# Performance work log

Measured on AMD Instinct MI355X. Metric: run time of the kernel, lower is better.

The kernel has to match this reference:

```python
import jax, jax.numpy as jnp
import numpy as np

B, N, D, H = 8, 1024, 768, 12
HD = D // H


def setup_inputs() -> dict:
    key = jax.random.key(0)
    ks = jax.random.split(key, 9)
    s = 1.0 / np.sqrt(D)
    return {
        "x": jax.random.normal(ks[0], (B, N, D), dtype=jnp.float32),
        "Wq": jax.random.normal(ks[1], (D, D), dtype=jnp.float32) * s,
        "bq": jax.random.normal(ks[2], (D,), dtype=jnp.float32) * 0.01,
        "Wk": jax.random.normal(ks[3], (D, D), dtype=jnp.float32) * s,
        "bk": jax.random.normal(ks[4], (D,), dtype=jnp.float32) * 0.01,
        "Wv": jax.random.normal(ks[5], (D, D), dtype=jnp.float32) * s,
        "bv": jax.random.normal(ks[6], (D,), dtype=jnp.float32) * 0.01,
        "Wo": jax.random.normal(ks[7], (D, D), dtype=jnp.float32) * s,
        "bo": jax.random.normal(ks[8], (D,), dtype=jnp.float32) * 0.01,
    }


def reference(x, Wq, bq, Wk, bk, Wv, bv, Wo, bo):
    b, n, d = x.shape
    split = lambda t: t.reshape(b, n, H, HD).transpose(0, 2, 1, 3)  # b h n d
    q = split(x @ Wq + bq)
    k = split(x @ Wk + bk)
    v = split(x @ Wv + bv)
    energy = jnp.einsum('bhqd,bhkd->bhqk', q, k)
    # NOTE: module scales AFTER softmax by sqrt(emb_size) (not head_dim) -- faithful.
    att = jax.nn.softmax(energy, axis=-1) / jnp.sqrt(jnp.float32(D)).astype(x.dtype)
    out = jnp.einsum('bhqk,bhkd->bhqd', att, v)
    out = out.transpose(0, 2, 1, 3).reshape(b, n, d)
    return out @ Wo + bo
```

## Files before the change

kernel.cpp:

```cpp
#include <hip/hip_runtime.h>

#define B_  8
#define N_  1024
#define D_  768
#define H_  12
#define HD_ 64
#define M_  (B_ * N_)
#define WELEM (D_ * D_)
#define XELEM ((size_t)M_ * D_)

typedef _Float16 f16;
typedef f16   f16x8  __attribute__((ext_vector_type(8)));
typedef short bf16x8 __attribute__((ext_vector_type(8)));
typedef float f32x4  __attribute__((ext_vector_type(4)));
typedef unsigned short u16;

__device__ __forceinline__ u16 f2bf(float f) {
    unsigned int x = __float_as_uint(f);
    return (u16)((x + 0x7fffu + ((x >> 16) & 1u)) >> 16);
}
__device__ __forceinline__ u16 f2h(float f) {
    return __builtin_bit_cast(u16, (f16)f);
}
__device__ __forceinline__ unsigned int cvtpk_bf16(float lo, float hi) {
    unsigned int r;
    asm("v_cvt_pk_bf16_f32 %0, %1, %2" : "=v"(r) : "v"(lo), "v"(hi));
    return r;
}
#if __has_builtin(__builtin_amdgcn_exp2f)
#define EXP2F(x) __builtin_amdgcn_exp2f(x)
#else
#define EXP2F(x) exp2f(x)
#endif

#define LOG2E_   1.4426950408889634f
#define EXPBIAS_ 28.853900817779268f

typedef __attribute__((address_space(3))) unsigned int       as3_u32;
typedef __attribute__((address_space(1))) const unsigned int as1_u32;
__device__ __forceinline__ void dma16(const void* g, void* l) {
    __builtin_amdgcn_global_load_lds((as1_u32*)g, (as3_u32*)l, 16, 0, 0);
}

__global__ __launch_bounds__(256) void cvt_x(const float* __restrict__ X,
                                             u16* __restrict__ Xh) {
    int idx = blockIdx.x * 256 + threadIdx.x;
    float4 v = ((const float4*)X)[idx];
    ushort4 o = {f2h(v.x), f2h(v.y), f2h(v.z), f2h(v.w)};
    ((ushort4*)Xh)[idx] = o;
}

__global__ __launch_bounds__(256) void cvt_w(
    const float* __restrict__ w0, const float* __restrict__ w1,
    const float* __restrict__ w2, const float* __restrict__ w3,
    u16* __restrict__ Wt) {
    const float* W = blockIdx.y == 0 ? w0 : blockIdx.y == 1 ? w1
                   : blockIdx.y == 2 ? w2 : w3;
    u16* dst = Wt + (size_t)blockIdx.y * WELEM;
    const int t  = threadIdx.x;
    const int tk = (blockIdx.x % 12) * 64, tn = (blockIdx.x / 12) * 64;
    __shared__ __align__(16) float tile[64][68];
#pragma unroll
    for (int i = 0; i < 4; ++i) {
        int r = (t >> 4) + i * 16, c4 = (t & 15) * 4;
        float4 v = *(const float4*)(W + (size_t)(tk + r) * D_ + tn + c4);
        *(float4*)&tile[r][c4] = v;
    }
    __syncthreads();
#pragma unroll
    for (int i = 0; i < 4; ++i) {
        int nr = (t >> 4) + i * 16, kc = (t & 15) * 4;
        ushort4 o = {f2h(tile[kc + 0][nr]), f2h(tile[kc + 1][nr]),
                     f2h(tile[kc + 2][nr]), f2h(tile[kc + 3][nr])};
        *(ushort4*)(dst + (size_t)(tn + nr) * D_ + tk + kc) = o;
    }
}

__global__ __launch_bounds__(256) void gemm_qkv(
    const u16* __restrict__ Xh, const u16* __restrict__ Wt,
    const float* __restrict__ bq, const float* __restrict__ bk,
    const float* __restrict__ bv, u16* __restrict__ Qf,
    u16* __restrict__ Kf, u16* __restrict__ Vt) {
    __shared__ __align__(16) u16 As[128 * 64];
    __shared__ __align__(16) u16 Bs[128 * 64];

    const int id  = blockIdx.x;
    const int xcd = id & 7, idx = id >> 3;
    const int m0  = (xcd * 8 + idx / 18) * 128;
    const int rem = idx % 18;
    const int z   = rem / 6, n0 = (rem % 6) * 128;

    const u16* Wz = Wt + (size_t)z * WELEM;
    const float* bias = z == 0 ? bq : z == 1 ? bk : bv;

    const int t = threadIdx.x, lane = t & 63, w = t >> 6;
    const int wm = w >> 1, wn = w & 1;
    const int quad = lane >> 4, ln = lane & 15;
    const int drow = lane >> 3, dcl = (lane & 7) ^ ((lane >> 3) & 7);

    f32x4 acc[4][4] = {};
    for (int k0 = 0; k0 < D_; k0 += 64) {
        __syncthreads();
#pragma unroll
        for (int j = 0; j < 4; ++j) {
            int i = w * 4 + j, row = i * 8 + drow;
            dma16(Xh + (size_t)(m0 + row) * D_ + k0 + dcl * 8, &As[i * 512]);
        }
#pragma unroll
        for (int j = 0; j < 4; ++j) {
            int i = w * 4 + j, row = i * 8 + drow;
            dma16(Wz + (size_t)(n0 + row) * D_ + k0 + dcl * 8, &Bs[i * 512]);
        }
        __syncthreads();
        f16x8 a[4][2], b[4][2];
#pragma unroll
        for (int mt = 0; mt < 4; ++mt)
#pragma unroll
            for (int ks = 0; ks < 2; ++ks)
                a[mt][ks] = *(const f16x8*)&As[(wm * 64 + mt * 16 + ln) * 64 +
                                               (((ks * 4 + quad) ^ (ln & 7)) * 8)];
#pragma unroll
        for (int nt = 0; nt < 4; ++nt)
#pragma unroll
            for (int ks = 0; ks < 2; ++ks)
                b[nt][ks] = *(const f16x8*)&Bs[(wn * 64 + nt * 16 + ln) * 64 +
                                               (((ks * 4 + quad) ^ (ln & 7)) * 8)];
#pragma unroll
        for (int mt = 0; mt < 4; ++mt)
#pragma unroll
            for (int nt = 0; nt < 4; ++nt) {
                acc[mt][nt] = __builtin_amdgcn_mfma_f32_16x16x32_f16(
                    a[mt][0], b[nt][0], acc[mt][nt], 0, 0, 0);
                acc[mt][nt] = __builtin_amdgcn_mfma_f32_16x16x32_f16(
                    a[mt][1], b[nt][1], acc[mt][nt], 0, 0, 0);
            }
    }
    const int h = (n0 >> 6) + wn;
#pragma unroll
    for (int nt = 0; nt < 4; ++nt) {
        int hd = nt * 16 + ln;
        float bv_ = bias[n0 + wn * 64 + hd];
#pragma unroll
        for (int mt = 0; mt < 4; ++mt) {
            int mb = m0 + wm * 64 + mt * 16 + quad * 4;
            int bb = mb >> 10, ns = mb & 1023;
            if (z == 0) {
#pragma unroll
                for (int r = 0; r < 4; ++r)
                    Qf[(((size_t)bb * H_ + h) * N_ + ns + r) * HD_ + hd] =
                        f2h((acc[mt][nt][r] + bv_) * LOG2E_);
            } else if (z == 1) {
#pragma unroll
                for (int r = 0; r < 4; ++r)
                    Kf[(((size_t)bb * H_ + h) * N_ + ns + r) * HD_ + hd] =
                        f2h(acc[mt][nt][r] + bv_);
            } else {
                ushort4 o = {f2bf(acc[mt][nt][0] + bv_), f2bf(acc[mt][nt][1] + bv_),
                             f2bf(acc[mt][nt][2] + bv_), f2bf(acc[mt][nt][3] + bv_)};
                *(ushort4*)(Vt + (((size_t)bb * H_ + h) * HD_ + hd) * N_ + ns) = o;
            }
        }
    }
}

__global__ __launch_bounds__(256) void attn_mfma(
    const u16* __restrict__ Qg, const u16* __restrict__ Kg,
    const u16* __restrict__ Vtg, u16* __restrict__ Og) {
    __shared__ __align__(16) u16 Ks[2][64 * 64];
    __shared__ __align__(16) u16 Vs[2][64 * 64];
    __shared__ __align__(16) u16 Ps[128 * 72];

    const int t = threadIdx.x, lane = t & 63, w = t >> 6;
    const int quad = lane >> 4, ln = lane & 15;
    const int drow = lane >> 3, dcl = (lane & 7) ^ ((lane >> 3) & 7);
    const int id  = blockIdx.x;
    const int id2 = (id & 7) * 96 + (id >> 3);
    const int bh  = id2 >> 3, qt = id2 & 7;
    const u16* Qh  = Qg  + ((size_t)bh * N_ + qt * 128) * HD_;
    const u16* Kh  = Kg  + (size_t)bh * N_ * HD_;
    const u16* Vth = Vtg + (size_t)bh * HD_ * N_;
    u16*       Oh  = Og  + ((size_t)bh * N_ + qt * 128) * HD_;

    const int rho0 = (w * 2 + 0) * 8 + drow;
    const int rho1 = (w * 2 + 1) * 8 + drow;
    const int gk0  = 4 * (rho0 & 15) + (rho0 >> 4);
    const int gk1  = 4 * (rho1 & 15) + (rho1 >> 4);

    f16x8 aq[2][2];
#pragma unroll
    for (int mt = 0; mt < 2; ++mt)
#pragma unroll
        for (int ks = 0; ks < 2; ++ks)
            aq[mt][ks] = *(const f16x8*)(Qh + (size_t)(w * 32 + mt * 16 + ln) * HD_ +
                                         ks * 32 + quad * 8);

    const bf16x8 pone = {0x3F80, 0x3F80, 0x3F80, 0x3F80,
                         0x3F80, 0x3F80, 0x3F80, 0x3F80};
    const f32x4 nb = {-EXPBIAS_, -EXPBIAS_, -EXPBIAS_, -EXPBIAS_};

    f32x4 oacc[2][4] = {};
    f32x4 lacc[2] = {};

    dma16(Kh + (size_t)gk0 * HD_ + dcl * 8, &Ks[0][(w * 2 + 0) * 512]);
    dma16(Kh + (size_t)gk1 * HD_ + dcl * 8, &Ks[0][(w * 2 + 1) * 512]);
    dma16(Vth + (size_t)rho0 * N_ + dcl * 8, &Vs[0][(w * 2 + 0) * 512]);
    dma16(Vth + (size_t)rho1 * N_ + dcl * 8, &Vs[0][(w * 2 + 1) * 512]);

#pragma unroll 2
    for (int kt = 0; kt < 16; ++kt) {
        const int cur = kt & 1;
        asm volatile("s_waitcnt vmcnt(0)" ::: "memory");
        __builtin_amdgcn_s_barrier();
        __builtin_amdgcn_sched_barrier(0);
        if (kt < 15) {
            const int nk = (kt + 1) * 64;
            dma16(Kh + (size_t)(nk + gk0) * HD_ + dcl * 8, &Ks[cur ^ 1][(w * 2 + 0) * 512]);
            dma16(Kh + (size_t)(nk + gk1) * HD_ + dcl * 8, &Ks[cur ^ 1][(w * 2 + 1) * 512]);
            dma16(Vth + (size_t)rho0 * N_ + nk + dcl * 8, &Vs[cur ^ 1][(w * 2 + 0) * 512]);
            dma16(Vth + (size_t)rho1 * N_ + nk + dcl * 8, &Vs[cur ^ 1][(w * 2 + 1) * 512]);
        }

        f32x4 sf[2][4];
        __builtin_amdgcn_s_setprio(1);
#pragma unroll
        for (int nt = 0; nt < 4; ++nt) {
            f16x8 b0 = *(const f16x8*)&Ks[cur][(nt * 16 + ln) * 64 + ((quad) ^ (ln & 7)) * 8];
            f16x8 b1 = *(const f16x8*)&Ks[cur][(nt * 16 + ln) * 64 + ((4 + quad) ^ (ln & 7)) * 8];
#pragma unroll
            for (int mt = 0; mt < 2; ++mt) {
                sf[mt][nt] = __builtin_amdgcn_mfma_f32_16x16x32_f16(aq[mt][0], b0, nb, 0, 0, 0);
                sf[mt][nt] = __builtin_amdgcn_mfma_f32_16x16x32_f16(aq[mt][1], b1, sf[mt][nt], 0, 0, 0);
            }
        }
        __builtin_amdgcn_s_setprio(0);

#pragma unroll
        for (int mt = 0; mt < 2; ++mt)
#pragma unroll
            for (int r = 0; r < 4; ++r) {
                float e0 = EXP2F(sf[mt][0][r]);
                float e1 = EXP2F(sf[mt][1][r]);
                float e2 = EXP2F(sf[mt][2][r]);
                float e3 = EXP2F(sf[mt][3][r]);
                uint2 pk;
                pk.x = cvtpk_bf16(e0, e1);
                pk.y = cvtpk_bf16(e2, e3);
                int q = w * 32 + mt * 16 + quad * 4 + r;
                *(uint2*)&Ps[q * 72 + ln * 4] = pk;
            }

        __builtin_amdgcn_s_setprio(1);
#pragma unroll
        for (int mt = 0; mt < 2; ++mt) {
            bf16x8 ap0 = *(const bf16x8*)&Ps[(w * 32 + mt * 16 + ln) * 72 + quad * 8];
            bf16x8 ap1 = *(const bf16x8*)&Ps[(w * 32 + mt * 16 + ln) * 72 + 32 + quad * 8];
            lacc[mt] = __builtin_amdgcn_mfma_f32_16x16x32_bf16(ap0, pone, lacc[mt], 0, 0, 0);
            lacc[mt] = __builtin_amdgcn_mfma_f32_16x16x32_bf16(ap1, pone, lacc[mt], 0, 0, 0);
#pragma unroll
            for (int nt = 0; nt < 4; ++nt) {
                bf16x8 bv0 = *(const bf16x8*)&Vs[cur][(nt * 16 + ln) * 64 +
                                                      ((quad ^ (ln & 7)) * 8)];
                oacc[mt][nt] = __builtin_amdgcn_mfma_f32_16x16x32_bf16(
                    ap0, bv0, oacc[mt][nt], 0, 0, 0);
                bf16x8 bv1 = *(const bf16x8*)&Vs[cur][(nt * 16 + ln) * 64 +
                                                      (((4 + quad) ^ (ln & 7)) * 8)];
                oacc[mt][nt] = __builtin_amdgcn_mfma_f32_16x16x32_bf16(
                    ap1, bv1, oacc[mt][nt], 0, 0, 0);
            }
        }
        __builtin_amdgcn_s_setprio(0);
    }

    const float sc = 0.036084391824351615f;
#pragma unroll
    for (int mt = 0; mt < 2; ++mt)
#pragma unroll
        for (int r = 0; r < 4; ++r) {
            float inv = sc / lacc[mt][r];
#pragma unroll
            for (int nt = 0; nt < 4; ++nt)
                Oh[(size_t)(w * 32 + mt * 16 + quad * 4 + r) * HD_ + nt * 16 + ln] =
                    f2h(oacc[mt][nt][r] * inv);
        }
}

__global__ __launch_bounds__(256) void gemm_out(
    const u16* __restrict__ Ob, const u16* __restrict__ Wto,
    const float* __restrict__ bias, float* __restrict__ Out) {
    __shared__ __align__(16) u16 As[128 * 64];
    __shared__ __align__(16) u16 Bs[64 * 64];

    const int id  = blockIdx.x;
    const int id2 = (id & 7) * 96 + (id >> 3);
    const int m0  = (id2 / 12) * 128, n0 = (id2 % 12) * 64;

    const int t = threadIdx.x, lane = t & 63, w = t >> 6;
    const int wm = w >> 1, wn = w & 1;
    const int quad = lane >> 4, ln = lane & 15;
    const int drow = lane >> 3, dcl = (lane & 7) ^ ((lane >> 3) & 7);

    f32x4 acc[4][2] = {};
    for (int k0 = 0; k0 < D_; k0 += 64) {
        int head = k0 >> 6;
        __syncthreads();
#pragma unroll
        for (int j = 0; j < 4; ++j) {
            int i = w * 4 + j, row = i * 8 + drow;
            int m = m0 + row, bb = m >> 10, ns = m & 1023;
            dma16(Ob + (((size_t)bb * H_ + head) * N_ + ns) * HD_ + dcl * 8, &As[i * 512]);
        }
#pragma unroll
        for (int j = 0; j < 2; ++j) {
            int i = w * 2 + j, row = i * 8 + drow;
            dma16(Wto + (size_t)(n0 + row) * D_ + k0 + dcl * 8, &Bs[i * 512]);
        }
        __syncthreads();
        f16x8 a[4][2], b[2][2];
#pragma unroll
        for (int mt = 0; mt < 4; ++mt)
#pragma unroll
            for (int ks = 0; ks < 2; ++ks)
                a[mt][ks] = *(const f16x8*)&As[(wm * 64 + mt * 16 + ln) * 64 +
                                               (((ks * 4 + quad) ^ (ln & 7)) * 8)];
#pragma unroll
        for (int nt = 0; nt < 2; ++nt)
#pragma unroll
            for (int ks = 0; ks < 2; ++ks)
                b[nt][ks] = *(const f16x8*)&Bs[(wn * 32 + nt * 16 + ln) * 64 +
                                               (((ks * 4 + quad) ^ (ln & 7)) * 8)];
#pragma unroll
        for (int mt = 0; mt < 4; ++mt)
#pragma unroll
            for (int nt = 0; nt < 2; ++nt) {
                acc[mt][nt] = __builtin_amdgcn_mfma_f32_16x16x32_f16(
                    a[mt][0], b[nt][0], acc[mt][nt], 0, 0, 0);
                acc[mt][nt] = __builtin_amdgcn_mfma_f32_16x16x32_f16(
                    a[mt][1], b[nt][1], acc[mt][nt], 0, 0, 0);
            }
    }
#pragma unroll
    for (int nt = 0; nt < 2; ++nt) {
        int n = n0 + wn * 32 + nt * 16 + ln;
        float bv_ = bias[n];
#pragma unroll
        for (int mt = 0; mt < 4; ++mt) {
            int mb = m0 + wm * 64 + mt * 16 + quad * 4;
#pragma unroll
            for (int r = 0; r < 4; ++r)
                Out[(size_t)(mb + r) * D_ + n] = acc[mt][nt][r] + bv_;
        }
    }
}

extern "C" void kernel_launch(void* const* d_in, const int* in_sizes, int n_in,
                              void* d_out, int out_size, void* d_ws, size_t ws_size,
                              hipStream_t stream) {
    const float* x  = (const float*)d_in[0];
    const float* Wq = (const float*)d_in[1];
    const float* bq = (const float*)d_in[2];
    const float* Wk = (const float*)d_in[3];
    const float* bk = (const float*)d_in[4];
    const float* Wv = (const float*)d_in[5];
    const float* bv = (const float*)d_in[6];
    const float* Wo = (const float*)d_in[7];
    const float* bo = (const float*)d_in[8];

    u16* Xh = (u16*)d_ws;
    u16* Wt = Xh + XELEM;
    u16* Qf = Wt + 4 * (size_t)WELEM;
    u16* Kf = Qf + XELEM;
    u16* Vt = Kf + XELEM;
    u16* Ob = Vt + XELEM;

    cvt_x<<<dim3((int)(XELEM / 4 / 256)), 256, 0, stream>>>(x, Xh);
    cvt_w<<<dim3(144, 4), 256, 0, stream>>>(Wq, Wk, Wv, Wo, Wt);
    gemm_qkv<<<dim3(1152), 256, 0, stream>>>(Xh, Wt, bq, bk, bv, Qf, Kf, Vt);
    attn_mfma<<<dim3(768), 256, 0, stream>>>(Qf, Kf, Vt, Ob);
    gemm_out<<<dim3(768), 256, 0, stream>>>(
        Ob, Wt + 3 * (size_t)WELEM, bo, (float*)d_out);
}
```

Measured before the change: 209.4 us.

## Double-buffer LDS tiles in projection GEMMs and shrink QKV N-tile

Both the QKV and output projection GEMMs now use two LDS buffers, issuing the next K-slice's async global-to-LDS loads before computing on the current one, with a single wait and barrier per iteration. This overlaps memory latency with MFMA work instead of serialising load and compute. The QKV GEMM also halves its N tile from 128 to 64, doubling the grid to 2304 blocks to keep LDS use per block similar and add parallelism. The trade-off is less data reuse per block and more redundant reads of X.

```diff
diff --git a/kernel.cpp b/kernel.cpp
--- a/kernel.cpp
+++ b/kernel.cpp
@@ -81,14 +81,14 @@
     const float* __restrict__ bq, const float* __restrict__ bk,
     const float* __restrict__ bv, u16* __restrict__ Qf,
     u16* __restrict__ Kf, u16* __restrict__ Vt) {
-    __shared__ __align__(16) u16 As[128 * 64];
-    __shared__ __align__(16) u16 Bs[128 * 64];
+    __shared__ __align__(16) u16 As[2][128 * 64];
+    __shared__ __align__(16) u16 Bs[2][64 * 64];
 
     const int id  = blockIdx.x;
     const int xcd = id & 7, idx = id >> 3;
-    const int m0  = (xcd * 8 + idx / 18) * 128;
-    const int rem = idx % 18;
-    const int z   = rem / 6, n0 = (rem % 6) * 128;
+    const int m0  = (xcd * 8 + idx / 36) * 128;
+    const int rem = idx % 36;
+    const int z   = rem / 12, n0 = (rem % 12) * 64;
 
     const u16* Wz = Wt + (size_t)z * WELEM;
     const float* bias = z == 0 ? bq : z == 1 ? bk : bv;
@@ -98,48 +98,67 @@
     const int quad = lane >> 4, ln = lane & 15;
     const int drow = lane >> 3, dcl = (lane & 7) ^ ((lane >> 3) & 7);
 
-    f32x4 acc[4][4] = {};
-    for (int k0 = 0; k0 < D_; k0 += 64) {
-        __syncthreads();
-#pragma unroll
-        for (int j = 0; j < 4; ++j) {
-            int i = w * 4 + j, row = i * 8 + drow;
-            dma16(Xh + (size_t)(m0 + row) * D_ + k0 + dcl * 8, &As[i * 512]);
-        }
-#pragma unroll
-        for (int j = 0; j < 4; ++j) {
-            int i = w * 4 + j, row = i * 8 + drow;
-            dma16(Wz + (size_t)(n0 + row) * D_ + k0 + dcl * 8, &Bs[i * 512]);
-        }
-        __syncthreads();
-        f16x8 a[4][2], b[4][2];
+#pragma unroll
+    for (int j = 0; j < 4; ++j) {
+        int i = w * 4 + j, row = i * 8 + drow;
+        dma16(Xh + (size_t)(m0 + row) * D_ + dcl * 8, &As[0][i * 512]);
+    }
+#pragma unroll
+    for (int j = 0; j < 2; ++j) {
+        int i = w * 2 + j, row = i * 8 + drow;
+        dma16(Wz + (size_t)(n0 + row) * D_ + dcl * 8, &Bs[0][i * 512]);
+    }
+
+    f32x4 acc[4][2] = {};
+#pragma unroll 2
+    for (int kk = 0; kk < 12; ++kk) {
+        const int cur = kk & 1;
+        asm volatile("s_waitcnt vmcnt(0)" ::: "memory");
+        __builtin_amdgcn_s_barrier();
+        __builtin_amdgcn_sched_barrier(0);
+        if (kk < 11) {
+            const int k1 = (kk + 1) * 64;
+#pragma unroll
+            for (int j = 0; j < 4; ++j) {
+                int i = w * 4 + j, row = i * 8 + drow;
+                dma16(Xh + (size_t)(m0 + row) * D_ + k1 + dcl * 8,
+                      &As[cur ^ 1][i * 512]);
+            }
+#pragma unroll
+            for (int j = 0; j < 2; ++j) {
+                int i = w * 2 + j, row = i * 8 + drow;
+                dma16(Wz + (size_t)(n0 + row) * D_ + k1 + dcl * 8,
+                      &Bs[cur ^ 1][i * 512]);
+            }
+        }
+        f16x8 a[4][2], b[2][2];
 #pragma unroll
         for (int mt = 0; mt < 4; ++mt)
 #pragma unroll
             for (int ks = 0; ks < 2; ++ks)
-                a[mt][ks] = *(const f16x8*)&As[(wm * 64 + mt * 16 + ln) * 64 +
-                                               (((ks * 4 + quad) ^ (ln & 7)) * 8)];
-#pragma unroll
-        for (int nt = 0; nt < 4; ++nt)
+                a[mt][ks] = *(const f16x8*)&As[cur][(wm * 64 + mt * 16 + ln) * 64 +
+                                                    (((ks * 4 + quad) ^ (ln & 7)) * 8)];
+#pragma unroll
+        for (int nt = 0; nt < 2; ++nt)
 #pragma unroll
             for (int ks = 0; ks < 2; ++ks)
-                b[nt][ks] = *(const f16x8*)&Bs[(wn * 64 + nt * 16 + ln) * 64 +
-                                               (((ks * 4 + quad) ^ (ln & 7)) * 8)];
+                b[nt][ks] = *(const f16x8*)&Bs[cur][(wn * 32 + nt * 16 + ln) * 64 +
+                                                    (((ks * 4 + quad) ^ (ln & 7)) * 8)];
 #pragma unroll
         for (int mt = 0; mt < 4; ++mt)
 #pragma unroll
-            for (int nt = 0; nt < 4; ++nt) {
+            for (int nt = 0; nt < 2; ++nt) {
                 acc[mt][nt] = __builtin_amdgcn_mfma_f32_16x16x32_f16(
                     a[mt][0], b[nt][0], acc[mt][nt], 0, 0, 0);
                 acc[mt][nt] = __builtin_amdgcn_mfma_f32_16x16x32_f16(
                     a[mt][1], b[nt][1], acc[mt][nt], 0, 0, 0);
             }
     }
-    const int h = (n0 >> 6) + wn;
-#pragma unroll
-    for (int nt = 0; nt < 4; ++nt) {
-        int hd = nt * 16 + ln;
-        float bv_ = bias[n0 + wn * 64 + hd];
+    const int h = n0 >> 6;
+#pragma unroll
+    for (int nt = 0; nt < 2; ++nt) {
+        int hd = wn * 32 + nt * 16 + ln;
+        float bv_ = bias[n0 + hd];
 #pragma unroll
         for (int mt = 0; mt < 4; ++mt) {
             int mb = m0 + wm * 64 + mt * 16 + quad * 4;
@@ -287,8 +306,8 @@
 __global__ __launch_bounds__(256) void gemm_out(
     const u16* __restrict__ Ob, const u16* __restrict__ Wto,
     const float* __restrict__ bias, float* __restrict__ Out) {
-    __shared__ __align__(16) u16 As[128 * 64];
-    __shared__ __align__(16) u16 Bs[64 * 64];
+    __shared__ __align__(16) u16 As[2][128 * 64];
+    __shared__ __align__(16) u16 Bs[2][64 * 64];
 
     const int id  = blockIdx.x;
     const int id2 = (id & 7) * 96 + (id >> 3);
@@ -299,35 +318,54 @@
     const int quad = lane >> 4, ln = lane & 15;
     const int drow = lane >> 3, dcl = (lane & 7) ^ ((lane >> 3) & 7);
 
+#pragma unroll
+    for (int j = 0; j < 4; ++j) {
+        int i = w * 4 + j, row = i * 8 + drow;
+        int m = m0 + row, bb = m >> 10, ns = m & 1023;
+        dma16(Ob + (((size_t)bb * H_ + 0) * N_ + ns) * HD_ + dcl * 8, &As[0][i * 512]);
+    }
+#pragma unroll
+    for (int j = 0; j < 2; ++j) {
+        int i = w * 2 + j, row = i * 8 + drow;
+        dma16(Wto + (size_t)(n0 + row) * D_ + dcl * 8, &Bs[0][i * 512]);
+    }
+
     f32x4 acc[4][2] = {};
-    for (int k0 = 0; k0 < D_; k0 += 64) {
-        int head = k0 >> 6;
-        __syncthreads();
-#pragma unroll
-        for (int j = 0; j < 4; ++j) {
-            int i = w * 4 + j, row = i * 8 + drow;
-            int m = m0 + row, bb = m >> 10, ns = m & 1023;
-            dma16(Ob + (((size_t)bb * H_ + head) * N_ + ns) * HD_ + dcl * 8, &As[i * 512]);
-        }
-#pragma unroll
-        for (int j = 0; j < 2; ++j) {
-            int i = w * 2 + j, row = i * 8 + drow;
-            dma16(Wto + (size_t)(n0 + row) * D_ + k0 + dcl * 8, &Bs[i * 512]);
-        }
-        __syncthreads();
+#pragma unroll 2
+    for (int kk = 0; kk < 12; ++kk) {
+        const int cur = kk & 1;
+        asm volatile("s_waitcnt vmcnt(0)" ::: "memory");
+        __builtin_amdgcn_s_barrier();
+        __builtin_amdgcn_sched_barrier(0);
+        if (kk < 11) {
+            const int head = kk + 1, k1 = head * 64;
+#pragma unroll
+            for (int j = 0; j < 4; ++j) {
+                int i = w * 4 + j, row = i * 8 + drow;
+                int m = m0 + row, bb = m >> 10, ns = m & 1023;
+                dma16(Ob + (((size_t)bb * H_ + head) * N_ + ns) * HD_ + dcl * 8,
+                      &As[cur ^ 1][i * 512]);
+            }
+#pragma unroll
+            for (int j = 0; j < 2; ++j) {
+                int i = w * 2 + j, row = i * 8 + drow;
+                dma16(Wto + (size_t)(n0 + row) * D_ + k1 + dcl * 8,
+                      &Bs[cur ^ 1][i * 512]);
+            }
+        }
         f16x8 a[4][2], b[2][2];
 #pragma unroll
         for (int mt = 0; mt < 4; ++mt)
 #pragma unroll
             for (int ks = 0; ks < 2; ++ks)
-                a[mt][ks] = *(const f16x8*)&As[(wm * 64 + mt * 16 + ln) * 64 +
-                                               (((ks * 4 + quad) ^ (ln & 7)) * 8)];
+                a[mt][ks] = *(const f16x8*)&As[cur][(wm * 64 + mt * 16 + ln) * 64 +
+                                                    (((ks * 4 + quad) ^ (ln & 7)) * 8)];
 #pragma unroll
         for (int nt = 0; nt < 2; ++nt)
 #pragma unroll
             for (int ks = 0; ks < 2; ++ks)
-                b[nt][ks] = *(const f16x8*)&Bs[(wn * 32 + nt * 16 + ln) * 64 +
-                                               (((ks * 4 + quad) ^ (ln & 7)) * 8)];
+                b[nt][ks] = *(const f16x8*)&Bs[cur][(wn * 32 + nt * 16 + ln) * 64 +
+                                                    (((ks * 4 + quad) ^ (ln & 7)) * 8)];
 #pragma unroll
         for (int mt = 0; mt < 4; ++mt)
 #pragma unroll
@@ -374,7 +412,7 @@
 
     cvt_x<<<dim3((int)(XELEM / 4 / 256)), 256, 0, stream>>>(x, Xh);
     cvt_w<<<dim3(144, 4), 256, 0, stream>>>(Wq, Wk, Wv, Wo, Wt);
-    gemm_qkv<<<dim3(1152), 256, 0, stream>>>(Xh, Wt, bq, bk, bv, Qf, Kf, Vt);
+    gemm_qkv<<<dim3(2304), 256, 0, stream>>>(Xh, Wt, bq, bk, bv, Qf, Kf, Vt);
     attn_mfma<<<dim3(768), 256, 0, stream>>>(Qf, Kf, Vt, Ob);
     gemm_out<<<dim3(768), 256, 0, stream>>>(
         Ob, Wt + 3 * (size_t)WELEM, bo, (float*)d_out);
```

New measurement: 199.4 us. 4.8% less time.
